# Performance work log

Measured on AMD Instinct MI355X. Metric: run time of the kernel, lower is better.

Reference implementation:

```python
import jax, jax.numpy as jnp
import numpy as np

K = 5  # filter_size
EPS = 1e-5

def conv1x1(x, w):
    # x: [B,Ci,H,W], w: [Co,Ci]
    return jnp.einsum('bihw,oi->bohw', x, w)

def layernorm_c(x, g, b):
    # LayerNorm over channel dim of NCHW (torch permutes to NHWC, norms last dim)
    m = x.mean(axis=1, keepdims=True)
    v = x.var(axis=1, keepdims=True)
    xn = (x - m) / jnp.sqrt(v + EPS)
    return xn * g[None, :, None, None] + b[None, :, None, None]

def conv3x3(x, w):
    return jax.lax.conv_general_dilated(x, w, (1, 1), [(1, 1), (1, 1)],
                                        dimension_numbers=('NCHW', 'OIHW', 'NCHW'))

def apply_dyn_filter(feat, filt):
    # feat: [B,C,H,W]; filt: [B,C*K*K,H,W] ordered as C x (K*K row-major), matching
    # torch .view(B,C,K*K,H,W) and F.unfold channel layout.
    B, C, H, W = feat.shape
    f = filt.reshape(B, C, K * K, H, W)
    p = K // 2
    fp = jnp.pad(feat, ((0, 0), (0, 0), (p, p), (p, p)))  # zero pad, same as F.unfold
    out = jnp.zeros_like(feat)
    for ki in range(K):
        for kj in range(K):
            out = out + fp[:, :, ki:ki + H, kj:kj + W] * f[:, :, ki * K + kj]
    return out


def setup_inputs() -> dict:
    key = jax.random.key(0)
    ks = jax.random.split(key, 9)
    B, Cin, H, W = 1, 64, 128, 128
    Ch = 128
    s = lambda fan: 1.0 / np.sqrt(fan)
    inp = {
        'rgb_high': jax.random.normal(ks[0], (B, Cin, H, W), jnp.float32),
        'event':    jax.random.normal(ks[1], (B, Cin, H, W), jnp.float32),
        'conv_w':   jax.random.normal(ks[2], (Ch, Cin), jnp.float32) * s(Cin),
        'ln_g':     jnp.ones((Ch,), jnp.float32),
        'ln_b':     jnp.zeros((Ch,), jnp.float32),
        'df1_w':    jax.random.normal(ks[3], (Ch, Ch, 3, 3), jnp.float32) * s(Ch * 9),
        'df2_w':    jax.random.normal(ks[4], (Ch * K * K, Ch), jnp.float32) * s(Ch),
        'sp_w':     jax.random.normal(ks[5], (Ch, Ch), jnp.float32) * s(Ch),
        'out_w':    jax.random.normal(ks[6], (Cin, Ch), jnp.float32) * s(Ch),
    }
    return inp


def reference(rgb_high, event, conv_w, ln_g, ln_b, df1_w, df2_w, sp_w, out_w):
    rgb_feat = layernorm_c(conv1x1(rgb_high, conv_w), ln_g, ln_b)
    ev_feat = layernorm_c(conv1x1(event, conv_w), ln_g, ln_b)
    # dynamic filter generator: conv3x3 -> ReLU -> conv1x1 (shared weights)
    rgb_filter = conv1x1(jax.nn.relu(conv3x3(rgb_feat, df1_w)), df2_w)
    ev_filter = conv1x1(jax.nn.relu(conv3x3(ev_feat, df1_w)), df2_w)
    rgb_en = apply_dyn_filter(rgb_feat, rgb_filter)
    ev_en = apply_dyn_filter(ev_feat, ev_filter)
    rgb_filtered = rgb_en * jax.nn.sigmoid(conv1x1(ev_en, sp_w))
    rgb_fused = rgb_en + rgb_filtered + rgb_feat
    rgb_norm = layernorm_c(rgb_fused, ln_g, ln_b)
    return conv1x1(rgb_norm, out_w)
```

## Files before the change

kernel.cpp:

```cpp
#include <hip/hip_runtime.h>
#include <math.h>

#define HW 16384
#define WD 128
#define HD 128
#define CIN 64
#define CH 128
#define EPSV 1e-5f

typedef __attribute__((ext_vector_type(8))) short short8;
typedef __attribute__((ext_vector_type(4))) short short4v;
typedef __attribute__((ext_vector_type(4))) float f32x4;

__device__ __forceinline__ short f2bf(float x) {
  unsigned u = __float_as_uint(x);
  u += 0x7FFFu + ((u >> 16) & 1u);
  return (short)(u >> 16);
}
__device__ __forceinline__ float bf2f(short x) {
  return __uint_as_float(((unsigned)(unsigned short)x) << 16);
}

__global__ __launch_bounds__(256) void k_prep_x(const float* __restrict__ rgb,
                                                const float* __restrict__ ev,
                                                short* __restrict__ xT_rgb,
                                                short* __restrict__ xT_ev) {
  const float* x = blockIdx.z ? ev : rgb;
  short* xT = blockIdx.z ? xT_ev : xT_rgb;
  int p = blockIdx.x * 256 + threadIdx.x;
#pragma unroll
  for (int cb = 0; cb < 8; ++cb) {
    short8 v;
#pragma unroll
    for (int j = 0; j < 8; ++j) v[j] = f2bf(x[(cb * 8 + j) * HW + p]);
    *(short8*)(xT + p * CIN + cb * 8) = v;
  }
}

__global__ __launch_bounds__(256) void k_prep_cw(const float* __restrict__ cw,
                                                 short* __restrict__ cwp) {
  int idx = blockIdx.x * 256 + threadIdx.x;
  int j = idx & 7, grp = (idx >> 3) & 3, m = (idx >> 5) & 127, q = idx >> 12;
  cwp[idx] = f2bf(cw[m * CIN + q * 32 + grp * 8 + j]);
}

__global__ __launch_bounds__(256) void k_prep_w3(const float* __restrict__ w3,
                                                 short* __restrict__ w3p) {
  int idx = blockIdx.x * 256 + threadIdx.x;
  int j = idx & 7, grp = (idx >> 3) & 3, m = (idx >> 5) & 127, ks = idx >> 12;
  int tap = ks >> 2, q = ks & 3;
  int c = q * 32 + grp * 8 + j;
  w3p[idx] = f2bf(w3[(m * CH + c) * 9 + tap]);
}

__global__ __launch_bounds__(256) void k_prep_df2(const float* __restrict__ df2,
                                                  short* __restrict__ df2p) {
  int idx = blockIdx.x * 256 + threadIdx.x;
  int j = idx & 7;
  int slotp = (idx >> 3) & 511;
  int c = idx >> 12;
  int t = slotp >> 4, k8l = slotp & 15;
  int k8 = k8l ^ (t & 7);
  float v = (t < 25) ? df2[(c * 25 + t) * CH + k8 * 8 + j] : 0.f;
  df2p[idx] = f2bf(v);
}

__global__ __launch_bounds__(256) void k_prep_spw(const float* __restrict__ spw,
                                                  short* __restrict__ spwp) {
  int idx = blockIdx.x * 256 + threadIdx.x;
  int j = idx & 7, grp = (idx >> 3) & 3, m = (idx >> 5) & 127, q = idx >> 12;
  spwp[idx] = f2bf(spw[m * CH + q * 32 + grp * 8 + j]);
}

__global__ __launch_bounds__(256) void k_prep_outw(const float* __restrict__ outw,
                                                   short* __restrict__ outwp) {
  int idx = blockIdx.x * 256 + threadIdx.x;
  int j = idx & 7, grp = (idx >> 3) & 3, m = (idx >> 5) & 63, q = idx >> 11;
  outwp[idx] = f2bf(outw[m * CH + q * 32 + grp * 8 + j]);
}

__global__ __launch_bounds__(256) void k_feat_mfma(
    const short* __restrict__ xT_rgb, const short* __restrict__ xT_ev,
    const short* __restrict__ cwp, const float* __restrict__ g,
    const float* __restrict__ b,
    short* __restrict__ featT_rgb, short* __restrict__ featT_ev) {
  __shared__ float sg[CH], sb[CH];
  int tid = threadIdx.x;
  if (tid < CH) { sg[tid] = g[tid]; sb[tid] = b[tid]; }
  __syncthreads();
  const short* xT = blockIdx.z ? xT_ev : xT_rgb;
  short* featT = blockIdx.z ? featT_ev : featT_rgb;
  int wave = tid >> 6, lane = tid & 63, col = lane & 15, grp = lane >> 4;
  int p = blockIdx.x * 64 + wave * 16 + col;

  const short8* bp = (const short8*)(xT + p * CIN);
  short8 bq0 = bp[grp], bq1 = bp[4 + grp];
  const short8* ap = (const short8*)cwp;

  f32x4 acc[8];
#pragma unroll
  for (int mt = 0; mt < 8; ++mt) {
    acc[mt] = (f32x4){0.f, 0.f, 0.f, 0.f};
    short8 a0 = ap[(0 * 128 + mt * 16 + col) * 4 + grp];
    short8 a1 = ap[(1 * 128 + mt * 16 + col) * 4 + grp];
    acc[mt] = __builtin_amdgcn_mfma_f32_16x16x32_bf16(a0, bq0, acc[mt], 0, 0, 0);
    acc[mt] = __builtin_amdgcn_mfma_f32_16x16x32_bf16(a1, bq1, acc[mt], 0, 0, 0);
  }
  float s = 0.f, s2 = 0.f;
#pragma unroll
  for (int mt = 0; mt < 8; ++mt)
#pragma unroll
    for (int r = 0; r < 4; ++r) { float v = acc[mt][r]; s += v; s2 += v * v; }
  s += __shfl_xor(s, 16);  s += __shfl_xor(s, 32);
  s2 += __shfl_xor(s2, 16); s2 += __shfl_xor(s2, 32);
  float mean = s * (1.f / CH);
  float var = s2 * (1.f / CH) - mean * mean;
  float rinv = rsqrtf(var + EPSV);
#pragma unroll
  for (int mt = 0; mt < 8; ++mt) {
    short4v fv;
#pragma unroll
    for (int r = 0; r < 4; ++r) {
      int m = mt * 16 + grp * 4 + r;
      fv[r] = f2bf((acc[mt][r] - mean) * rinv * sg[m] + sb[m]);
    }
    *(short4v*)(featT + p * CH + mt * 16 + grp * 4) = fv;
  }
}

__global__ __launch_bounds__(256) void k_conv3_v2(
    const short* __restrict__ featT_rgb, const short* __restrict__ featT_ev,
    const short* __restrict__ w3p,
    short* __restrict__ rT_rgb, short* __restrict__ rT_ev) {
  const short* featT = blockIdx.z ? featT_ev : featT_rgb;
  short* rT = blockIdx.z ? rT_ev : rT_rgb;
  int tid = threadIdx.x, wave = tid >> 6, lane = tid & 63;
  int col = lane & 15, grp = lane >> 4;
  int mh = wave & 1;
  int ty = (blockIdx.x >> 3) * 4 + (wave >> 1) * 2;
  int tx = (blockIdx.x & 7) * 16;
  int x = tx + col;

  f32x4 acc[2][4];
#pragma unroll
  for (int s = 0; s < 2; ++s)
#pragma unroll
    for (int mt = 0; mt < 4; ++mt) acc[s][mt] = (f32x4){0.f, 0.f, 0.f, 0.f};

  const short8* ap = (const short8*)w3p;
  for (int ks = 0; ks < 36; ++ks) {
    int tap = ks >> 2, q = ks & 3;
    int dy = tap / 3 - 1, dx = tap % 3 - 1;
    int xs = x + dx;
    bool xok = (unsigned)xs < (unsigned)WD;
    int y0 = ty + dy, y1 = ty + 1 + dy;
    short8 b0 = {0, 0, 0, 0, 0, 0, 0, 0}, b1 = {0, 0, 0, 0, 0, 0, 0, 0};
    if (xok && (unsigned)y0 < (unsigned)HD)
      b0 = *(const short8*)(featT + (y0 * WD + xs) * CH + q * 32 + grp * 8);
    if (xok && (unsigned)y1 < (unsigned)HD)
      b1 = *(const short8*)(featT + (y1 * WD + xs) * CH + q * 32 + grp * 8);
#pragma unroll
    for (int mt = 0; mt < 4; ++mt) {
      short8 a = ap[(ks * 128 + (mh * 4 + mt) * 16 + col) * 4 + grp];
      acc[0][mt] = __builtin_amdgcn_mfma_f32_16x16x32_bf16(a, b0, acc[0][mt], 0, 0, 0);
      acc[1][mt] = __builtin_amdgcn_mfma_f32_16x16x32_bf16(a, b1, acc[1][mt], 0, 0, 0);
    }
  }
#pragma unroll
  for (int s = 0; s < 2; ++s) {
    int p = (ty + s) * WD + x;
#pragma unroll
    for (int mt = 0; mt < 4; ++mt) {
      short4v v;
#pragma unroll
      for (int r = 0; r < 4; ++r) v[r] = f2bf(fmaxf(acc[s][mt][r], 0.f));
      *(short4v*)(rT + p * CH + (mh * 4 + mt) * 16 + grp * 4) = v;
    }
  }
}

__global__ __launch_bounds__(256, 3) void k_filt_v6(
    const short* __restrict__ featT_rgb, const short* __restrict__ featT_ev,
    const short* __restrict__ rT_rgb, const short* __restrict__ rT_ev,
    const short* __restrict__ df2p,
    short* __restrict__ enT_rgb, short* __restrict__ enT_ev) {
  __shared__ short lsA[4 * 512 * 8];
  __shared__ float fwv[4 * 400 + 64];
  const short* featT = blockIdx.z ? featT_ev : featT_rgb;
  const short* rT = blockIdx.z ? rT_ev : rT_rgb;
  short* enT = blockIdx.z ? enT_ev : enT_rgb;
  int tid = threadIdx.x;
  int wave = tid >> 6, lane = tid & 63;
  int col = lane & 15, grp = lane >> 4;
  int ty0 = (blockIdx.x >> 3) * 16, tx0 = (blockIdx.x & 7) * 16;
  int c0 = blockIdx.y * 4;
  int py0 = ty0 + wave * 4;
  int pxx = tx0 + col;

  {
    const short8* gsrc = (const short8*)(df2p + (size_t)c0 * 4096);
    short8* lA = (short8*)lsA;
    for (int i = tid; i < 2048; i += 256) lA[i] = gsrc[i];
  }
  for (int px = tid; px < 400; px += 256) {
    int wr = px / 20, wc = px % 20;
    int y = ty0 + wr - 2, x = tx0 + wc - 2;
    short4v v = {0, 0, 0, 0};
    if ((unsigned)y < (unsigned)HD && (unsigned)x < (unsigned)WD)
      v = *(const short4v*)(featT + (y * WD + x) * CH + c0);
#pragma unroll
    for (int ci = 0; ci < 4; ++ci) fwv[ci * 400 + px] = bf2f(v[ci]);
  }
  if (tid < 64) fwv[4 * 400 + tid] = 0.f;

  short8 rv[4][4];
#pragma unroll
  for (int s = 0; s < 4; ++s) {
    const short8* bp = (const short8*)(rT + ((py0 + s) * WD + pxx) * CH);
#pragma unroll
    for (int q = 0; q < 4; ++q) rv[s][q] = bp[q * 4 + grp];
  }
#pragma unroll
  for (int s = 0; s < 4; ++s)
#pragma unroll
    for (int q = 0; q < 4; ++q) asm volatile("" :: "v"(rv[s][q]));

  int idx0[4], idx1[4];
#pragma unroll
  for (int r = 0; r < 4; ++r) {
    int tap0 = grp * 4 + r;
    int tap1 = 16 + grp * 4 + r;
    idx0[r] = (wave * 4 + tap0 / 5) * 20 + col + tap0 % 5;
    idx1[r] = (wave * 4 + tap1 / 5) * 20 + col + tap1 % 5;
  }
  __syncthreads();

  const short8* lA8 = (const short8*)lsA;
  int sw = (grp << 2) ^ (col & 7);
  short* stp = enT + ((py0 + grp) * WD + pxx) * CH + c0;
  short4v sv;

#pragma unroll
  for (int c = 0; c < 4; ++c) {
    int base0 = c * 512 + col * 16;
    int base1 = base0 + 256;
    short8 a[4];
    f32x4 acc0[4], acc1[4];
#pragma unroll
    for (int q = 0; q < 4; ++q) a[q] = lA8[base0 + ((q << 2) ^ sw ^ (grp << 2) ^ grp) ];
#pragma unroll
    for (int q = 0; q < 4; ++q) a[q] = lA8[base0 + (((q << 2) | grp) ^ (col & 7))];
#pragma unroll
    for (int s = 0; s < 4; ++s) {
      acc0[s] = (f32x4){0.f, 0.f, 0.f, 0.f};
#pragma unroll
      for (int q = 0; q < 4; ++q)
        acc0[s] = __builtin_amdgcn_mfma_f32_16x16x32_bf16(a[q], rv[s][q], acc0[s], 0, 0, 0);
    }
#pragma unroll
    for (int q = 0; q < 4; ++q) a[q] = lA8[base1 + (((q << 2) | grp) ^ (col & 7))];
#pragma unroll
    for (int s = 0; s < 4; ++s) {
      acc1[s] = (f32x4){0.f, 0.f, 0.f, 0.f};
#pragma unroll
      for (int q = 0; q < 4; ++q)
        acc1[s] = __builtin_amdgcn_mfma_f32_16x16x32_bf16(a[q], rv[s][q], acc1[s], 0, 0, 0);
    }
    const float* fwc = fwv + c * 400;
    float part[4];
#pragma unroll
    for (int s = 0; s < 4; ++s) {
      float p = 0.f;
#pragma unroll
      for (int r = 0; r < 4; ++r) {
        p += fwc[idx0[r] + s * 20] * acc0[s][r];
        p += fwc[idx1[r] + s * 20] * acc1[s][r];
      }
      part[s] = p;
    }
#pragma unroll
    for (int s = 0; s < 4; ++s) part[s] += __shfl_xor(part[s], 16);
#pragma unroll
    for (int s = 0; s < 4; ++s) part[s] += __shfl_xor(part[s], 32);
    float val = (grp == 0) ? part[0] : (grp == 1) ? part[1]
              : (grp == 2) ? part[2] : part[3];
    sv[c] = f2bf(val);
  }
  *(short4v*)stp = sv;
}

__global__ __launch_bounds__(256) void k_post(
    const short* __restrict__ enT_rgb, const short* __restrict__ enT_ev,
    const short* __restrict__ featT_rgb,
    const short* __restrict__ spwp, const short* __restrict__ outwp,
    const float* __restrict__ g, const float* __restrict__ b,
    float* __restrict__ out) {
  __shared__ short nlds[4][16 * 136];
  __shared__ float sg[CH], sb[CH];
  int tid = threadIdx.x;
  if (tid < CH) { sg[tid] = g[tid]; sb[tid] = b[tid]; }
  __syncthreads();
  int wave = tid >> 6, lane = tid & 63, col = lane & 15, grp = lane >> 4;
  int p = blockIdx.x * 64 + wave * 16 + col;

  const short8* bp = (const short8*)(enT_ev + p * CH);
  short8 bq[4];
#pragma unroll
  for (int q = 0; q < 4; ++q) bq[q] = bp[q * 4 + grp];
  const short8* ap = (const short8*)spwp;
  f32x4 z[8];
#pragma unroll
  for (int mt = 0; mt < 8; ++mt) {
    z[mt] = (f32x4){0.f, 0.f, 0.f, 0.f};
#pragma unroll
    for (int q = 0; q < 4; ++q)
      z[mt] = __builtin_amdgcn_mfma_f32_16x16x32_bf16(
          ap[(q * 128 + mt * 16 + col) * 4 + grp], bq[q], z[mt], 0, 0, 0);
  }

  const short4v* er = (const short4v*)(enT_rgb + p * CH);
  const short4v* fr = (const short4v*)(featT_rgb + p * CH);
  float fused[8][4];
  float s = 0.f, s2 = 0.f;
#pragma unroll
  for (int mt = 0; mt < 8; ++mt) {
    short4v e4 = er[mt * 4 + grp];
    short4v f4 = fr[mt * 4 + grp];
#pragma unroll
    for (int r = 0; r < 4; ++r) {
      float sig = 1.f / (1.f + __expf(-z[mt][r]));
      float f = bf2f(e4[r]) * (1.f + sig) + bf2f(f4[r]);
      fused[mt][r] = f; s += f; s2 += f * f;
    }
  }
  s += __shfl_xor(s, 16);  s += __shfl_xor(s, 32);
  s2 += __shfl_xor(s2, 16); s2 += __shfl_xor(s2, 32);
  float mean = s * (1.f / CH);
  float var = s2 * (1.f / CH) - mean * mean;
  float rinv = rsqrtf(var + EPSV);

  short* nl = &nlds[wave][0];
#pragma unroll
  for (int mt = 0; mt < 8; ++mt) {
    short4v nv;
#pragma unroll
    for (int r = 0; r < 4; ++r) {
      int o = mt * 16 + grp * 4 + r;
      nv[r] = f2bf((fused[mt][r] - mean) * rinv * sg[o] + sb[o]);
    }
    *(short4v*)(nl + col * 136 + mt * 16 + grp * 4) = nv;
  }

  short8 nb[4];
#pragma unroll
  for (int q = 0; q < 4; ++q)
    nb[q] = *(const short8*)(nl + col * 136 + q * 32 + grp * 8);
  const short8* op = (const short8*)outwp;
#pragma unroll
  for (int mt = 0; mt < 4; ++mt) {
    f32x4 oacc = {0.f, 0.f, 0.f, 0.f};
#pragma unroll
    for (int q = 0; q < 4; ++q)
      oacc = __builtin_amdgcn_mfma_f32_16x16x32_bf16(
          op[(q * 64 + mt * 16 + col) * 4 + grp], nb[q], oacc, 0, 0, 0);
#pragma unroll
    for (int r = 0; r < 4; ++r)
      out[(mt * 16 + grp * 4 + r) * HW + p] = oacc[r];
  }
}

extern "C" void kernel_launch(void* const* d_in, const int* in_sizes, int n_in,
                              void* d_out, int out_size, void* d_ws, size_t ws_size,
                              hipStream_t stream) {
  const float* rgb  = (const float*)d_in[0];
  const float* ev   = (const float*)d_in[1];
  const float* cw   = (const float*)d_in[2];
  const float* g    = (const float*)d_in[3];
  const float* b    = (const float*)d_in[4];
  const float* w3   = (const float*)d_in[5];
  const float* df2  = (const float*)d_in[6];
  const float* spw  = (const float*)d_in[7];
  const float* outw = (const float*)d_in[8];
  float* out = (float*)d_out;
  char* wsb = (char*)d_ws;

  const size_t MB = 1u << 20;
  short* featT_rgb = (short*)(wsb);
  short* featT_ev  = (short*)(wsb + 4 * MB);
  short* rT_rgb    = (short*)(wsb + 8 * MB);
  short* rT_ev     = (short*)(wsb + 12 * MB);
  short* enT_rgb   = (short*)(wsb + 16 * MB);
  short* enT_ev    = (short*)(wsb + 20 * MB);
  short* xT_rgb    = (short*)(wsb + 24 * MB);
  short* xT_ev     = (short*)(wsb + 26 * MB);
  short* df2p      = (short*)(wsb + 28 * MB);
  short* w3p       = (short*)(wsb + 29 * MB);
  short* cwp       = (short*)(wsb + 30 * MB);
  short* spwp      = (short*)(wsb + 31 * MB);
  short* outwp     = (short*)(wsb + 32 * MB);

  hipLaunchKernelGGL(k_prep_x, dim3(64, 1, 2), dim3(256), 0, stream,
                     rgb, ev, xT_rgb, xT_ev);
  hipLaunchKernelGGL(k_prep_cw, dim3(32), dim3(256), 0, stream, cw, cwp);
  hipLaunchKernelGGL(k_prep_w3, dim3(576), dim3(256), 0, stream, w3, w3p);
  hipLaunchKernelGGL(k_prep_df2, dim3(2048), dim3(256), 0, stream, df2, df2p);
  hipLaunchKernelGGL(k_prep_spw, dim3(64), dim3(256), 0, stream, spw, spwp);
  hipLaunchKernelGGL(k_prep_outw, dim3(32), dim3(256), 0, stream, outw, outwp);
  hipLaunchKernelGGL(k_feat_mfma, dim3(256, 1, 2), dim3(256), 0, stream,
                     xT_rgb, xT_ev, cwp, g, b, featT_rgb, featT_ev);
  hipLaunchKernelGGL(k_conv3_v2, dim3(256, 1, 2), dim3(256), 0, stream,
                     featT_rgb, featT_ev, w3p, rT_rgb, rT_ev);
  hipLaunchKernelGGL(k_filt_v6, dim3(64, 32, 2), dim3(256), 0, stream,
                     featT_rgb, featT_ev, rT_rgb, rT_ev, df2p, enT_rgb, enT_ev);
  hipLaunchKernelGGL(k_post, dim3(256), dim3(256), 0, stream,
                     enT_rgb, enT_ev, featT_rgb, spwp, outwp, g, b, out);
}
```

Baseline: 124.4 us.

## Reorder dynamic-filter taps for contiguous LDS weight reads and unroll conv3 loop

The df2 weight packing is rearranged so that each MFMA row group maps to a row of filter taps (or, for the second tile, a column of taps). This lets each lane read its four feature-window values from contiguous LDS addresses. A transposed copy of the feature window is kept in shared memory to serve the column-ordered taps, and the per-lane index arrays are replaced by a base offset plus a stride. The 36-iteration conv3x3 loop is also fully unrolled so tap offsets become compile-time constants, at the cost of more LDS, more code size and possible register pressure.

```diff
diff --git a/kernel.cpp b/kernel.cpp
--- a/kernel.cpp
+++ b/kernel.cpp
@@ -57,11 +57,19 @@
                                                   short* __restrict__ df2p) {
   int idx = blockIdx.x * 256 + threadIdx.x;
   int j = idx & 7;
-  int slotp = (idx >> 3) & 511;
+  int k8s = (idx >> 3) & 15;
+  int m = (idx >> 7) & 31;
   int c = idx >> 12;
-  int t = slotp >> 4, k8l = slotp & 15;
-  int k8 = k8l ^ (t & 7);
-  float v = (t < 25) ? df2[(c * 25 + t) * CH + k8 * 8 + j] : 0.f;
+  int k8 = k8s ^ (m & 7);
+  int k = k8 * 8 + j;
+  int grp = (m >> 2) & 3, r = m & 3;
+  int t;
+  if (m < 16) t = grp * 5 + r;
+  else if (grp == 0) t = 20 + r;
+  else if (grp == 1) t = r * 5 + 4;
+  else if (grp == 2 && r == 0) t = 24;
+  else t = -1;
+  float v = (t >= 0) ? df2[(c * 25 + t) * CH + k] : 0.f;
   df2p[idx] = f2bf(v);
 }
 
@@ -128,7 +136,7 @@
   }
 }
 
-__global__ __launch_bounds__(256) void k_conv3_v2(
+__global__ __launch_bounds__(256) void k_conv3_v3(
     const short* __restrict__ featT_rgb, const short* __restrict__ featT_ev,
     const short* __restrict__ w3p,
     short* __restrict__ rT_rgb, short* __restrict__ rT_ev) {
@@ -148,9 +156,10 @@
     for (int mt = 0; mt < 4; ++mt) acc[s][mt] = (f32x4){0.f, 0.f, 0.f, 0.f};
 
   const short8* ap = (const short8*)w3p;
+#pragma unroll
   for (int ks = 0; ks < 36; ++ks) {
-    int tap = ks >> 2, q = ks & 3;
-    int dy = tap / 3 - 1, dx = tap % 3 - 1;
+    const int tap = ks >> 2, q = ks & 3;
+    const int dy = tap / 3 - 1, dx = tap % 3 - 1;
     int xs = x + dx;
     bool xok = (unsigned)xs < (unsigned)WD;
     int y0 = ty + dy, y1 = ty + 1 + dy;
@@ -179,13 +188,13 @@
   }
 }
 
-__global__ __launch_bounds__(256, 3) void k_filt_v6(
+__global__ __launch_bounds__(256, 3) void k_filt_v7(
     const short* __restrict__ featT_rgb, const short* __restrict__ featT_ev,
     const short* __restrict__ rT_rgb, const short* __restrict__ rT_ev,
     const short* __restrict__ df2p,
     short* __restrict__ enT_rgb, short* __restrict__ enT_ev) {
   __shared__ short lsA[4 * 512 * 8];
-  __shared__ float fwv[4 * 400 + 64];
+  __shared__ float fwall[2 * 4 * 408];
   const short* featT = blockIdx.z ? featT_ev : featT_rgb;
   const short* rT = blockIdx.z ? rT_ev : rT_rgb;
   short* enT = blockIdx.z ? enT_ev : enT_rgb;
@@ -209,9 +218,17 @@
     if ((unsigned)y < (unsigned)HD && (unsigned)x < (unsigned)WD)
       v = *(const short4v*)(featT + (y * WD + x) * CH + c0);
 #pragma unroll
-    for (int ci = 0; ci < 4; ++ci) fwv[ci * 400 + px] = bf2f(v[ci]);
-  }
-  if (tid < 64) fwv[4 * 400 + tid] = 0.f;
+    for (int ci = 0; ci < 4; ++ci) {
+      float f = bf2f(v[ci]);
+      fwall[ci * 408 + wr * 20 + wc] = f;
+      fwall[4 * 408 + ci * 408 + wc * 20 + wr] = f;
+    }
+  }
+  if (tid < 64) {
+    int ci = tid >> 4, k = tid & 7;
+    if ((tid & 8) == 0) fwall[ci * 408 + 400 + k] = 0.f;
+    else fwall[4 * 408 + ci * 408 + 400 + k] = 0.f;
+  }
 
   short8 rv[4][4];
 #pragma unroll
@@ -225,18 +242,16 @@
 #pragma unroll
     for (int q = 0; q < 4; ++q) asm volatile("" :: "v"(rv[s][q]));
 
-  int idx0[4], idx1[4];
-#pragma unroll
-  for (int r = 0; r < 4; ++r) {
-    int tap0 = grp * 4 + r;
-    int tap1 = 16 + grp * 4 + r;
-    idx0[r] = (wave * 4 + tap0 / 5) * 20 + col + tap0 % 5;
-    idx1[r] = (wave * 4 + tap1 / 5) * 20 + col + tap1 % 5;
-  }
+  int rowb = wave * 4;
+  int off0 = (rowb + grp) * 20 + col;
+  int off1, step1;
+  if (grp == 0)      { off1 = (rowb + 4) * 20 + col;            step1 = 20; }
+  else if (grp == 1) { off1 = 4 * 408 + (col + 4) * 20 + rowb;  step1 = 1;  }
+  else if (grp == 2) { off1 = (rowb + 4) * 20 + col + 4;        step1 = 20; }
+  else               { off1 = 0;                                step1 = 0;  }
   __syncthreads();
 
   const short8* lA8 = (const short8*)lsA;
-  int sw = (grp << 2) ^ (col & 7);
   short* stp = enT + ((py0 + grp) * WD + pxx) * CH + c0;
   short4v sv;
 
@@ -247,8 +262,6 @@
     short8 a[4];
     f32x4 acc0[4], acc1[4];
 #pragma unroll
-    for (int q = 0; q < 4; ++q) a[q] = lA8[base0 + ((q << 2) ^ sw ^ (grp << 2) ^ grp) ];
-#pragma unroll
     for (int q = 0; q < 4; ++q) a[q] = lA8[base0 + (((q << 2) | grp) ^ (col & 7))];
 #pragma unroll
     for (int s = 0; s < 4; ++s) {
@@ -266,16 +279,17 @@
       for (int q = 0; q < 4; ++q)
         acc1[s] = __builtin_amdgcn_mfma_f32_16x16x32_bf16(a[q], rv[s][q], acc1[s], 0, 0, 0);
     }
-    const float* fwc = fwv + c * 400;
+    const float* fw_c = fwall + c * 408;
     float part[4];
 #pragma unroll
     for (int s = 0; s < 4; ++s) {
+      const float* f0 = fw_c + off0 + s * 20;
+      const float* f1 = fwall + c * 408 + off1 + s * step1;
       float p = 0.f;
 #pragma unroll
-      for (int r = 0; r < 4; ++r) {
-        p += fwc[idx0[r] + s * 20] * acc0[s][r];
-        p += fwc[idx1[r] + s * 20] * acc1[s][r];
-      }
+      for (int r = 0; r < 4; ++r) p += f0[r] * acc0[s][r];
+#pragma unroll
+      for (int r = 0; r < 4; ++r) p += f1[r] * acc1[s][r];
       part[s] = p;
     }
 #pragma unroll
@@ -408,9 +422,9 @@
   hipLaunchKernelGGL(k_prep_outw, dim3(32), dim3(256), 0, stream, outw, outwp);
   hipLaunchKernelGGL(k_feat_mfma, dim3(256, 1, 2), dim3(256), 0, stream,
                      xT_rgb, xT_ev, cwp, g, b, featT_rgb, featT_ev);
-  hipLaunchKernelGGL(k_conv3_v2, dim3(256, 1, 2), dim3(256), 0, stream,
+  hipLaunchKernelGGL(k_conv3_v3, dim3(256, 1, 2), dim3(256), 0, stream,
                      featT_rgb, featT_ev, w3p, rT_rgb, rT_ev);
-  hipLaunchKernelGGL(k_filt_v6, dim3(64, 32, 2), dim3(256), 0, stream,
+  hipLaunchKernelGGL(k_filt_v7, dim3(64, 32, 2), dim3(256), 0, stream,
                      featT_rgb, featT_ev, rT_rgb, rT_ev, df2p, enT_rgb, enT_ev);
   hipLaunchKernelGGL(k_post, dim3(256), dim3(256), 0, stream,
                      enT_rgb, enT_ev, featT_rgb, spwp, outwp, g, b, out);
```

Result: slower. 156.2 us (+25.6%).
